# Optimization experiments

Measured on AMD Instinct MI355X. Metric: run time of the kernel, lower is better.

Reference implementation:

```python
import jax, jax.numpy as jnp
import numpy as np

N = 10000      # nodes
E = 160000     # edges
C = 72         # hidden dim = 18 * mul (mul=4)
A = 16         # node_attr dim (16x0e)
L = 3          # layers
O = 64         # output dim (64x0e)
B = 16         # graphs in batch
IN_DIM = 18    # irreps_node_input dim
SH = 9         # spherical harmonics dim, lmax=2
FC = 100       # radial MLP hidden (fc_neurons=[1,100])
MAX_RADIUS = 2.0
NUM_NEIGHBORS = 16.0
NUM_NODES = 625.0


def sph_harm_l2(d):
    # component-normalized real spherical harmonics up to l=2 on unit vectors d [E,3]
    x, y, z = d[:, 0], d[:, 1], d[:, 2]
    s3, s5, s15 = 3.0 ** 0.5, 5.0 ** 0.5, 15.0 ** 0.5
    return jnp.stack([
        jnp.ones_like(x),
        s3 * x, s3 * y, s3 * z,
        s15 * x * y, s15 * y * z, (s5 / 2.0) * (3.0 * z * z - 1.0),
        s15 * x * z, (s15 / 2.0) * (x * x - y * y),
    ], axis=1)  # [E, 9]


def setup_inputs() -> dict:
    key = jax.random.key(0)
    ks = jax.random.split(key, 16)
    pos = jax.random.normal(ks[0], (N, 3), dtype=jnp.float32)
    node_attr = jax.random.normal(ks[1], (N, A), dtype=jnp.float32)
    batch = jnp.sort(jax.random.randint(ks[2], (N,), 0, B))
    edge_src = jax.random.randint(ks[3], (E,), 0, N)
    edge_dst = jax.random.randint(ks[4], (E,), 0, N)
    W_in = jax.random.normal(ks[5], (IN_DIM, C), dtype=jnp.float32) / np.sqrt(IN_DIM)
    W_tp = jax.random.normal(ks[6], (L, SH, C, C), dtype=jnp.float32) / np.sqrt(C)
    W_self = jax.random.normal(ks[7], (L, C, C), dtype=jnp.float32) / np.sqrt(C)
    W_attr = jax.random.normal(ks[8], (L, A, C), dtype=jnp.float32) / np.sqrt(A)
    fc1_w = jax.random.normal(ks[9], (L, 1, FC), dtype=jnp.float32)
    fc1_b = jnp.zeros((L, FC), dtype=jnp.float32)
    fc2_w = jax.random.normal(ks[10], (L, FC, SH), dtype=jnp.float32) / np.sqrt(FC)
    W_out = jax.random.normal(ks[11], (C, O), dtype=jnp.float32) / np.sqrt(C)
    return {"pos": pos, "node_attr": node_attr, "batch": batch,
            "edge_src": edge_src, "edge_dst": edge_dst,
            "W_in": W_in, "W_tp": W_tp, "W_self": W_self, "W_attr": W_attr,
            "fc1_w": fc1_w, "fc1_b": fc1_b, "fc2_w": fc2_w, "W_out": W_out}


def reference(pos, node_attr, batch, edge_src, edge_dst,
              W_in, W_tp, W_self, W_attr, fc1_w, fc1_b, fc2_w, W_out):
    n = pos.shape[0]
    # edge geometry
    rvec = pos[edge_src] - pos[edge_dst]                      # [E,3]
    r = jnp.linalg.norm(rvec, axis=1, keepdims=True)          # [E,1]
    dvec = rvec / jnp.maximum(r, 1e-9)
    sh = sph_harm_l2(dvec)                                    # [E,9]
    # single cosine radial basis with cutoff at max_radius (number_of_basis=1)
    t = r / MAX_RADIUS
    emb = jnp.where(t < 1.0, jnp.cos(0.5 * jnp.pi * t), 0.0)  # [E,1]
    # node inputs: fixed one-hot on the scalar channel, embedded to hidden dim
    onehot = jnp.zeros((IN_DIM,), dtype=pos.dtype).at[0].set(1.0)
    h = jnp.broadcast_to((onehot @ W_in)[None, :], (n, C))    # [N,C]
    for l in range(L):
        # radial MLP -> per-edge, per-SH-path weights
        u = jax.nn.silu(emb @ fc1_w[l] + fc1_b[l]) @ fc2_w[l]  # [E,9]
        path = u * sh                                          # [E,9]
        hs = h[edge_src]                                       # [E,C]
        m = jnp.zeros_like(hs)
        for s in range(SH):  # fixed small set of tensor-product paths
            m = m + path[:, s:s + 1] * (hs @ W_tp[l, s])       # [E,C]
        agg = jax.ops.segment_sum(m, edge_dst, num_segments=n) / np.sqrt(NUM_NEIGHBORS)
        h = jax.nn.gelu(agg + h @ W_self[l] + node_attr @ W_attr[l])
    out_nodes = h @ W_out                                      # [N,O]
    pooled = jax.ops.segment_sum(out_nodes, batch, num_segments=B)
    return pooled / np.sqrt(NUM_NODES)                         # [B,O]
```

## Files before the change

kernel.cpp:

```cpp
#include <hip/hip_runtime.h>
#include <math.h>

#define NN 10000
#define NE 160000
#define CC 72
#define AA 16
#define LL 3
#define OO 64
#define NBATCH 16
#define SH 9
#define FCN 100
#define KK (SH*CC)
#define KA 736
#define KP 768
#define KG 96
#define NT 5
#define PSTRIDE 12
#define NB 1024

typedef __attribute__((ext_vector_type(8))) short bf16x8;
typedef __attribute__((ext_vector_type(4))) float f32x4;

static __device__ __forceinline__ float gelu_tanh(float x) {
    float x3 = x * x * x;
    float inner = 0.7978845608028654f * (x + 0.044715f * x3);
    return 0.5f * x * (1.0f + tanhf(inner));
}
static __device__ __forceinline__ unsigned short f2bf(float x) {
    unsigned int u = __float_as_uint(x);
    u += 0x7FFFu + ((u >> 16) & 1u);
    return (unsigned short)(u >> 16);
}

__global__ void k_hist(const float* __restrict__ pos, const int* __restrict__ esrc,
                       const int* __restrict__ edst, int* __restrict__ cnt) {
    int e = blockIdx.x * blockDim.x + threadIdx.x;
    if (e >= NE) return;
    int s = esrc[e], d = edst[e];
    float dx = pos[3 * s] - pos[3 * d];
    float dy = pos[3 * s + 1] - pos[3 * d + 1];
    float dz = pos[3 * s + 2] - pos[3 * d + 2];
    float r = sqrtf(dx * dx + dy * dy + dz * dz);
    if (r * 0.5f < 1.0f) atomicAdd(&cnt[d], 1);
}

__global__ void k_scan(const int* __restrict__ cnt, int* __restrict__ off) {
    __shared__ int sa[256], sb[256];
    const int PER = 40;
    int t = threadIdx.x;
    int base = t * PER;
    int loc[PER];
    int run = 0;
#pragma unroll
    for (int i = 0; i < PER; ++i) {
        int idx = base + i;
        int v = (idx < NN) ? cnt[idx] : 0;
        loc[i] = run;
        run += v;
    }
    sa[t] = run;
    __syncthreads();
    int* in = sa; int* out = sb;
    for (int o = 1; o < 256; o <<= 1) {
        int v = in[t];
        if (t >= o) v += in[t - o];
        out[t] = v;
        __syncthreads();
        int* tmp = in; in = out; out = tmp;
    }
    int ebase = (t > 0) ? in[t - 1] : 0;
#pragma unroll
    for (int i = 0; i < PER; ++i) {
        int idx = base + i;
        if (idx <= NN) off[idx] = ebase + loc[i];
    }
}

__global__ void k_scatter2(const float* __restrict__ pos, const int* __restrict__ esrc,
                           const int* __restrict__ edst, const int* __restrict__ off,
                           int* __restrict__ cur, int* __restrict__ src_s,
                           int* __restrict__ dst_s) {
    int e = blockIdx.x * blockDim.x + threadIdx.x;
    if (e >= NE) return;
    int s = esrc[e], d = edst[e];
    float dx = pos[3 * s] - pos[3 * d];
    float dy = pos[3 * s + 1] - pos[3 * d + 1];
    float dz = pos[3 * s + 2] - pos[3 * d + 2];
    float r = sqrtf(dx * dx + dy * dy + dz * dz);
    if (r * 0.5f < 1.0f) {
        int slot = off[d] + atomicAdd(&cur[d], 1);
        src_s[slot] = s;
        dst_s[slot] = d;
    }
}

__global__ void k_utab(const float* __restrict__ fc1w, const float* __restrict__ fc1b,
                       const float* __restrict__ fc2w, float* __restrict__ U) {
    int i = blockIdx.x * blockDim.x + threadIdx.x;
    if (i >= LL * (NB + 1)) return;
    int l = i / (NB + 1), b = i - l * (NB + 1);
    float emb = cosf(1.5707963267948966f * ((float)b / (float)NB));
    float u[SH];
#pragma unroll
    for (int q = 0; q < SH; ++q) u[q] = 0.f;
    const float* w1 = &fc1w[l * FCN];
    const float* b1 = &fc1b[l * FCN];
    const float* w2 = &fc2w[l * FCN * SH];
    for (int f = 0; f < FCN; ++f) {
        float a = emb * w1[f] + b1[f];
        float si = a / (1.0f + expf(-a));
#pragma unroll
        for (int q = 0; q < SH; ++q) u[q] += si * w2[f * SH + q];
    }
    float* ud = &U[(size_t)i * 12];
#pragma unroll
    for (int q = 0; q < SH; ++q) ud[q] = u[q];
    ud[9] = 0.f; ud[10] = 0.f; ud[11] = 0.f;
}

__global__ __launch_bounds__(256) void k_path2(const float* __restrict__ pos,
                                               const int* __restrict__ src_s,
                                               const int* __restrict__ dst_s,
                                               const float* __restrict__ U,
                                               const int* __restrict__ off,
                                               float* __restrict__ path) {
    int slot = blockIdx.x * blockDim.x + threadIdx.x;
    if (slot >= off[NN]) return;
    int s = src_s[slot], d = dst_s[slot];
    float dx = pos[3 * s] - pos[3 * d];
    float dy = pos[3 * s + 1] - pos[3 * d + 1];
    float dz = pos[3 * s + 2] - pos[3 * d + 2];
    float r = sqrtf(dx * dx + dy * dy + dz * dz);
    float inv = 1.0f / fmaxf(r, 1e-9f);
    float x = dx * inv, y = dy * inv, z = dz * inv;
    const float s3 = 1.7320508075688772f;
    const float s5 = 2.23606797749979f;
    const float s15 = 3.872983346207417f;
    float sh[SH];
    sh[0] = 1.0f;
    sh[1] = s3 * x;
    sh[2] = s3 * y;
    sh[3] = s3 * z;
    sh[4] = s15 * x * y;
    sh[5] = s15 * y * z;
    sh[6] = 0.5f * s5 * (3.0f * z * z - 1.0f);
    sh[7] = s15 * x * z;
    sh[8] = 0.5f * s15 * (x * x - y * y);

    float fb = r * 0.5f * (float)NB;
    int b0 = (int)fb;
    float fr = fb - (float)b0;

#pragma unroll
    for (int l = 0; l < LL; ++l) {
        const float* t0 = &U[((size_t)l * (NB + 1) + b0) * 12];
        float4 a0 = *(const float4*)(t0 + 0);
        float4 a1 = *(const float4*)(t0 + 4);
        float  a2 = t0[8];
        float4 c0 = *(const float4*)(t0 + 12);
        float4 c1 = *(const float4*)(t0 + 16);
        float  c2 = t0[20];
        float u0 = a0.x + fr * (c0.x - a0.x);
        float u1 = a0.y + fr * (c0.y - a0.y);
        float u2 = a0.z + fr * (c0.z - a0.z);
        float u3 = a0.w + fr * (c0.w - a0.w);
        float u4 = a1.x + fr * (c1.x - a1.x);
        float u5 = a1.y + fr * (c1.y - a1.y);
        float u6 = a1.z + fr * (c1.z - a1.z);
        float u7 = a1.w + fr * (c1.w - a1.w);
        float u8 = a2   + fr * (c2   - a2);
        float* pd = &path[((size_t)l * NE + slot) * PSTRIDE];
        *(float4*)(pd + 0) = make_float4(u0 * sh[0], u1 * sh[1], u2 * sh[2], u3 * sh[3]);
        *(float4*)(pd + 4) = make_float4(u4 * sh[4], u5 * sh[5], u6 * sh[6], u7 * sh[7]);
        *(float4*)(pd + 8) = make_float4(u8 * sh[8], 0.f, 0.f, 0.f);
    }
}

__global__ void k_init(const float* __restrict__ W_in, float* __restrict__ h) {
    int i = blockIdx.x * blockDim.x + threadIdx.x;
    if (i < NN * CC) h[i] = W_in[i % CC];
}

__global__ void k_wcat2(const float* __restrict__ Wtp, const float* __restrict__ Wself,
                        const float* __restrict__ Wattr, unsigned short* __restrict__ Wb) {
    int i = blockIdx.x * blockDim.x + threadIdx.x;
    if (i >= LL * NT * KG * 128) return;
    int l = i / (NT * KG * 128);
    int rem = i - l * (NT * KG * 128);
    int nt = rem / (KG * 128); rem -= nt * (KG * 128);
    int kg = rem / 128; int e = rem - kg * 128;
    int n = nt * 16 + (e >> 3);
    int k = kg * 8 + (e & 7);
    float v = 0.f;
    if (n < CC && k < KA) {
        if (k < KK)            v = 0.25f * Wtp[(size_t)l * KK * CC + k * CC + n];
        else if (k < KK + CC)  v = Wself[(size_t)l * CC * CC + (k - KK) * CC + n];
        else                   v = Wattr[(size_t)l * AA * CC + (k - KK - CC) * CC + n];
    }
    Wb[i] = f2bf(v);
}

__global__ __launch_bounds__(1024) void k_layer(const float* __restrict__ h,
                                                const float* __restrict__ attr,
                                                const float* __restrict__ path_l,
                                                const int* __restrict__ src_s,
                                                const int* __restrict__ off,
                                                const unsigned short* __restrict__ Wb,
                                                float* __restrict__ hout) {
    __shared__ unsigned short Alds[KG * 128];
    __shared__ float red[3 * NT * 64 * 4];
    int t = threadIdx.x, w = t >> 6, lane = t & 63;
    int n0 = blockIdx.x * 16;
    int d = n0 + w;

    float a1[SH], a2[SH];
#pragma unroll
    for (int q = 0; q < SH; ++q) { a1[q] = 0.f; a2[q] = 0.f; }
    int b = off[d], e = off[d + 1];
    bool two = lane < (CC - 64);
    for (int i = b; i < e; ++i) {
        int s = src_s[i];
        float hv1 = h[(size_t)s * CC + lane];
        float hv2 = two ? h[(size_t)s * CC + 64 + lane] : 0.f;
        const float* p = &path_l[(size_t)i * PSTRIDE];
        float4 p0 = *(const float4*)p;
        float4 p1 = *(const float4*)(p + 4);
        float p8 = p[8];
        a1[0] += p0.x * hv1; a2[0] += p0.x * hv2;
        a1[1] += p0.y * hv1; a2[1] += p0.y * hv2;
        a1[2] += p0.z * hv1; a2[2] += p0.z * hv2;
        a1[3] += p0.w * hv1; a2[3] += p0.w * hv2;
        a1[4] += p1.x * hv1; a2[4] += p1.x * hv2;
        a1[5] += p1.y * hv1; a2[5] += p1.y * hv2;
        a1[6] += p1.z * hv1; a2[6] += p1.z * hv2;
        a1[7] += p1.w * hv1; a2[7] += p1.w * hv2;
        a1[8] += p8 * hv1;   a2[8] += p8 * hv2;
    }
    unsigned short* At = Alds + w * 8;
    int kgc = lane >> 3, kjc = lane & 7;
#pragma unroll
    for (int q = 0; q < SH; ++q) {
        At[(9 * q + kgc) * 128 + kjc] = f2bf(a1[q]);
        if (two) At[(9 * q + 8) * 128 + lane] = f2bf(a2[q]);
    }
    At[(81 + kgc) * 128 + kjc] = f2bf(h[(size_t)d * CC + lane]);
    if (two) At[89 * 128 + lane] = f2bf(h[(size_t)d * CC + 64 + lane]);
    if (lane < AA) At[(90 + (lane >> 3)) * 128 + (lane & 7)] = f2bf(attr[(size_t)d * AA + lane]);
    if (lane < 32) At[(92 + (lane >> 3)) * 128 + (lane & 7)] = 0;
    __syncthreads();

    if (w < 4) {
        const unsigned short* Ab = Alds + (lane & 15) * 8;
        const unsigned short* Bb = Wb + (lane & 15) * 8;
        f32x4 acc[NT];
#pragma unroll
        for (int nt = 0; nt < NT; ++nt) acc[nt] = (f32x4){0.f, 0.f, 0.f, 0.f};
        int s0 = w * 6;
#pragma unroll
        for (int s = 0; s < 6; ++s) {
            int kg = (s0 + s) * 4 + (lane >> 4);
            bf16x8 af = *(const bf16x8*)(Ab + (size_t)kg * 128);
#pragma unroll
            for (int nt = 0; nt < NT; ++nt) {
                bf16x8 bf = *(const bf16x8*)(Bb + ((size_t)nt * KG + kg) * 128);
                acc[nt] = __builtin_amdgcn_mfma_f32_16x16x32_bf16(af, bf, acc[nt], 0, 0, 0);
            }
        }
        if (w) {
#pragma unroll
            for (int nt = 0; nt < NT; ++nt)
                *(f32x4*)&red[(((w - 1) * NT + nt) * 64 + lane) * 4] = acc[nt];
        }
        __syncthreads();
        if (w == 0) {
            int cb = lane & 15, rb = (lane >> 4) * 4;
            int row = n0 + rb;
#pragma unroll
            for (int nt = 0; nt < NT; ++nt) {
                f32x4 p0 = *(const f32x4*)&red[((0 * NT + nt) * 64 + lane) * 4];
                f32x4 p1 = *(const f32x4*)&red[((1 * NT + nt) * 64 + lane) * 4];
                f32x4 p2 = *(const f32x4*)&red[((2 * NT + nt) * 64 + lane) * 4];
                int col = nt * 16 + cb;
                if (col < CC) {
#pragma unroll
                    for (int j = 0; j < 4; ++j) {
                        float v = acc[nt][j] + p0[j] + p1[j] + p2[j];
                        hout[(size_t)(row + j) * CC + col] = gelu_tanh(v);
                    }
                }
            }
        }
    } else {
        __syncthreads();
    }
}

__global__ __launch_bounds__(256) void k_pool(const float* __restrict__ h,
                                              const int* __restrict__ batch,
                                              float* __restrict__ hp) {
    __shared__ float sp[NBATCH * CC];
    int t = threadIdx.x;
    for (int i = t; i < NBATCH * CC; i += 256) sp[i] = 0.f;
    __syncthreads();
    int n0 = blockIdx.x * 16;
    for (int i = t; i < 16 * CC; i += 256) {
        int nl = i / CC, c = i - nl * CC;
        int n = n0 + nl;
        if (n < NN) atomicAdd(&sp[batch[n] * CC + c], h[(size_t)n * CC + c]);
    }
    __syncthreads();
    for (int i = t; i < NBATCH * CC; i += 256) {
        float v = sp[i];
        if (v != 0.f) atomicAdd(&hp[i], v);
    }
}

__global__ __launch_bounds__(1024) void k_outmm(const float* __restrict__ hp,
                                                const float* __restrict__ Wout,
                                                float* __restrict__ out) {
    __shared__ float hs[NBATCH * CC];
    int t = threadIdx.x;
    for (int i = t; i < NBATCH * CC; i += 1024) hs[i] = hp[i];
    __syncthreads();
    int b = t >> 6, o = t & 63;
    float acc = 0.f;
#pragma unroll 8
    for (int c = 0; c < CC; ++c) acc += hs[b * CC + c] * Wout[c * OO + o];
    out[t] = acc * (1.0f / 25.0f);
}

extern "C" void kernel_launch(void* const* d_in, const int* in_sizes, int n_in,
                              void* d_out, int out_size, void* d_ws, size_t ws_size,
                              hipStream_t stream) {
    const float* pos       = (const float*)d_in[0];
    const float* node_attr = (const float*)d_in[1];
    const int*   batch     = (const int*)d_in[2];
    const int*   esrc      = (const int*)d_in[3];
    const int*   edst      = (const int*)d_in[4];
    const float* W_in      = (const float*)d_in[5];
    const float* W_tp      = (const float*)d_in[6];
    const float* W_self    = (const float*)d_in[7];
    const float* W_attr    = (const float*)d_in[8];
    const float* fc1w      = (const float*)d_in[9];
    const float* fc1b      = (const float*)d_in[10];
    const float* fc2w      = (const float*)d_in[11];
    const float* W_out     = (const float*)d_in[12];
    float* out = (float*)d_out;

    char* p = (char*)d_ws;
    auto alloc = [&](size_t bytes) -> void* {
        void* r = (void*)p;
        p += (bytes + 255) & ~(size_t)255;
        return r;
    };
    int*   cnt   = (int*)alloc((size_t)NN * 4);
    int*   cur   = (int*)alloc((size_t)NN * 4);
    int*   off   = (int*)alloc((size_t)(NN + 1) * 4);
    int*   src_s = (int*)alloc((size_t)NE * 4);
    int*   dst_s = (int*)alloc((size_t)NE * 4);
    float* path  = (float*)alloc((size_t)LL * NE * PSTRIDE * 4);
    float* U     = (float*)alloc((size_t)LL * (NB + 1) * 12 * 4);
    unsigned short* Wb = (unsigned short*)alloc((size_t)LL * NT * KG * 128 * 2);
    float* h0    = (float*)alloc((size_t)NN * CC * 4);
    float* h1    = (float*)alloc((size_t)NN * CC * 4);
    float* hp    = (float*)alloc((size_t)NBATCH * CC * 4);

    hipMemsetAsync(cnt, 0, (size_t)NN * 4, stream);
    hipMemsetAsync(cur, 0, (size_t)NN * 4, stream);
    hipMemsetAsync(hp, 0, (size_t)NBATCH * CC * 4, stream);

    k_hist<<<(NE + 255) / 256, 256, 0, stream>>>(pos, esrc, edst, cnt);
    k_utab<<<(LL * (NB + 1) + 255) / 256, 256, 0, stream>>>(fc1w, fc1b, fc2w, U);
    k_wcat2<<<(LL * NT * KG * 128 + 255) / 256, 256, 0, stream>>>(W_tp, W_self, W_attr, Wb);
    k_init<<<(NN * CC + 255) / 256, 256, 0, stream>>>(W_in, h0);
    k_scan<<<1, 256, 0, stream>>>(cnt, off);
    k_scatter2<<<(NE + 255) / 256, 256, 0, stream>>>(pos, esrc, edst, off, cur, src_s, dst_s);
    k_path2<<<(NE + 255) / 256, 256, 0, stream>>>(pos, src_s, dst_s, U, off, path);

    const float* hin = h0;
    float* hout = h1;
    for (int l = 0; l < LL; ++l) {
        k_layer<<<NN / 16, 1024, 0, stream>>>(hin, node_attr,
                                              path + (size_t)l * NE * PSTRIDE, src_s, off,
                                              Wb + (size_t)l * NT * KG * 128, hout);
        const float* tmp = hin; hin = hout; hout = (float*)tmp;
    }
    k_pool<<<(NN + 15) / 16, 256, 0, stream>>>(hin, batch, hp);
    k_outmm<<<1, 1024, 0, stream>>>(hp, W_out, out);
}
```

Before: 166.0 us.

## Stage gathered neighbor features and path weights in LDS per block

Instead of each wavefront serially gathering its destination node's source rows from global memory, the whole 1024-thread block cooperatively loads chunks of up to 176 edges (source indices, path coefficients and gathered h rows) into shared memory. Each wave then accumulates from LDS. This turns a per-wave serial dependent gather into a block-wide parallel load, exposing more memory-level parallelism. The cost is extra block-wide barriers and a large LDS footprint, roughly 50KB added, which may reduce occupancy.

```diff
diff --git a/kernel.cpp b/kernel.cpp
--- a/kernel.cpp
+++ b/kernel.cpp
@@ -17,6 +17,7 @@
 #define NT 5
 #define PSTRIDE 12
 #define NB 1024
+#define EMAX 176
 
 typedef __attribute__((ext_vector_type(8))) short bf16x8;
 typedef __attribute__((ext_vector_type(4))) float f32x4;
@@ -207,35 +208,57 @@
                                                 const int* __restrict__ off,
                                                 const unsigned short* __restrict__ Wb,
                                                 float* __restrict__ hout) {
+    __shared__ float Hlds[EMAX * CC];
+    __shared__ float Plds[EMAX * PSTRIDE];
+    __shared__ int   Slds[EMAX];
     __shared__ unsigned short Alds[KG * 128];
     __shared__ float red[3 * NT * 64 * 4];
     int t = threadIdx.x, w = t >> 6, lane = t & 63;
     int n0 = blockIdx.x * 16;
     int d = n0 + w;
+    int b0 = off[n0], e0 = off[n0 + 16];
+    int db = off[d], de = off[d + 1];
 
     float a1[SH], a2[SH];
 #pragma unroll
     for (int q = 0; q < SH; ++q) { a1[q] = 0.f; a2[q] = 0.f; }
-    int b = off[d], e = off[d + 1];
     bool two = lane < (CC - 64);
-    for (int i = b; i < e; ++i) {
-        int s = src_s[i];
-        float hv1 = h[(size_t)s * CC + lane];
-        float hv2 = two ? h[(size_t)s * CC + 64 + lane] : 0.f;
-        const float* p = &path_l[(size_t)i * PSTRIDE];
-        float4 p0 = *(const float4*)p;
-        float4 p1 = *(const float4*)(p + 4);
-        float p8 = p[8];
-        a1[0] += p0.x * hv1; a2[0] += p0.x * hv2;
-        a1[1] += p0.y * hv1; a2[1] += p0.y * hv2;
-        a1[2] += p0.z * hv1; a2[2] += p0.z * hv2;
-        a1[3] += p0.w * hv1; a2[3] += p0.w * hv2;
-        a1[4] += p1.x * hv1; a2[4] += p1.x * hv2;
-        a1[5] += p1.y * hv1; a2[5] += p1.y * hv2;
-        a1[6] += p1.z * hv1; a2[6] += p1.z * hv2;
-        a1[7] += p1.w * hv1; a2[7] += p1.w * hv2;
-        a1[8] += p8 * hv1;   a2[8] += p8 * hv2;
-    }
+
+    for (int base = b0; base < e0; base += EMAX) {
+        int nE = min(EMAX, e0 - base);
+        if (t < nE) Slds[t] = src_s[base + t];
+        for (int idx = t; idx < nE * PSTRIDE; idx += 1024)
+            Plds[idx] = path_l[(size_t)base * PSTRIDE + idx];
+        __syncthreads();
+        for (int idx = t; idx < nE * CC; idx += 1024) {
+            int e = idx / CC, c = idx - e * CC;
+            Hlds[idx] = h[(size_t)Slds[e] * CC + c];
+        }
+        __syncthreads();
+        int lb = db > base ? db : base;
+        int le = de < base + nE ? de : base + nE;
+        for (int i = lb; i < le; ++i) {
+            int eL = i - base;
+            const float* hr = &Hlds[eL * CC];
+            float hv1 = hr[lane];
+            float hv2 = two ? hr[64 + lane] : 0.f;
+            const float* p = &Plds[eL * PSTRIDE];
+            float4 p0 = *(const float4*)p;
+            float4 p1 = *(const float4*)(p + 4);
+            float p8 = p[8];
+            a1[0] += p0.x * hv1; a2[0] += p0.x * hv2;
+            a1[1] += p0.y * hv1; a2[1] += p0.y * hv2;
+            a1[2] += p0.z * hv1; a2[2] += p0.z * hv2;
+            a1[3] += p0.w * hv1; a2[3] += p0.w * hv2;
+            a1[4] += p1.x * hv1; a2[4] += p1.x * hv2;
+            a1[5] += p1.y * hv1; a2[5] += p1.y * hv2;
+            a1[6] += p1.z * hv1; a2[6] += p1.z * hv2;
+            a1[7] += p1.w * hv1; a2[7] += p1.w * hv2;
+            a1[8] += p8 * hv1;   a2[8] += p8 * hv2;
+        }
+        __syncthreads();
+    }
+
     unsigned short* At = Alds + w * 8;
     int kgc = lane >> 3, kjc = lane & 7;
 #pragma unroll
```

New measurement: 181.2 us. +9.1%, slower.
